# Performance work log

Hardware: AMD Instinct MI355X
Metric: run time of the kernel (lower is better)

The kernel has to match this reference:

```python
import jax, jax.numpy as jnp
import numpy as np

PARTS = (0.0, 0.25, 0.5, 0.75, 1.0)
N = 16777216


def setup_inputs() -> dict:
    key = jax.random.key(0)
    kx, ky, kd = jax.random.split(key, 3)
    x = jax.random.normal(kx, (N, 2), dtype=jnp.float32)
    y = jax.random.normal(ky, (N, 2), dtype=jnp.float32)
    dist = jax.random.uniform(kd, (N,), dtype=jnp.float32)
    return {"x": x, "y": y, "dist": dist}


def _complex_abs(v):
    # fastmri.complex_abs: sqrt(re^2 + im^2) over last dim of size 2
    return jnp.sqrt(jnp.sum(v * v, axis=-1))


def reference(x, y, dist):
    # Per-element squared errors computed once, then masked-reduced per radial bin.
    diff2_sum = jnp.sum((x - y) ** 2, axis=-1)        # [N] sum over the 2 components
    abs_diff2 = (_complex_abs(x) - _complex_abs(y)) ** 2  # [N]

    loss = jnp.float32(0.0)
    for i in range(len(PARTS) - 1):
        r0, r1 = PARTS[i], PARTS[i + 1]
        mask = (dist >= r0) & (dist <= r1)            # inclusive both ends, as in torch code
        cnt = jnp.sum(mask)                           # number of selected points
        # mse over x[ind] of shape [cnt, 2] -> divide by 2*cnt elements
        mse = jnp.sum(jnp.where(mask, diff2_sum, 0.0)) / jnp.maximum(2 * cnt, 1)
        mse_abs = jnp.sum(jnp.where(mask, abs_diff2, 0.0)) / jnp.maximum(cnt, 1)
        loss = loss + jnp.where(cnt > 0, mse + 0.1 * mse_abs, 0.0)
    return loss
```

## Files before the change

kernel.cpp:

```cpp
#include <hip/hip_runtime.h>

#define NBINS 4
#define BLOCK 256
#define WAVES_PER_BLOCK (BLOCK / 64)
#define NBLOCKS 2048

struct WS {
    float sum_v[NBINS];
    float cnt[NBINS];
};

__device__ __forceinline__ void accum_point(float x0, float x1, float y0, float y1,
                                            float d,
                                            float (&acc)[NBINS], float (&cnt)[NBINS]) {
    float sx = fmaf(x1, x1, x0 * x0);
    float sy = fmaf(y1, y1, y0 * y0);
    float dx0 = x0 - y0, dx1 = x1 - y1;
    float d2 = fmaf(dx1, dx1, dx0 * dx0);
    float t = __builtin_amdgcn_sqrtf(sx * sy);
    float ad2 = sx + sy - 2.0f * t;
    float v = fmaf(0.1f, ad2, 0.5f * d2);
    bool c1 = d < 0.25f;
    bool c2 = d < 0.5f;
    bool c3 = d < 0.75f;
    float m0 = c1 ? 1.0f : 0.0f;
    float m1 = (c2 && !c1) ? 1.0f : 0.0f;
    float m2 = (c3 && !c2) ? 1.0f : 0.0f;
    float m3 = c3 ? 0.0f : 1.0f;
    acc[0] = fmaf(v, m0, acc[0]);
    acc[1] = fmaf(v, m1, acc[1]);
    acc[2] = fmaf(v, m2, acc[2]);
    acc[3] = fmaf(v, m3, acc[3]);
    cnt[0] += m0;
    cnt[1] += m1;
    cnt[2] += m2;
    cnt[3] += m3;
}

__device__ __forceinline__ void accum2(const float4& xv, const float4& yv,
                                       const float2& dv,
                                       float (&acc)[NBINS], float (&cnt)[NBINS]) {
    accum_point(xv.x, xv.y, yv.x, yv.y, dv.x, acc, cnt);
    accum_point(xv.z, xv.w, yv.z, yv.w, dv.y, acc, cnt);
}

__global__ __launch_bounds__(BLOCK, 4) void radial_loss_main(
    const float* __restrict__ x, const float* __restrict__ y,
    const float* __restrict__ dist, WS* __restrict__ ws, int n) {
    float acc[NBINS] = {0.f, 0.f, 0.f, 0.f};
    float cnt[NBINS] = {0.f, 0.f, 0.f, 0.f};

    const int n2 = n >> 1;
    const float4* __restrict__ x4 = (const float4*)x;
    const float4* __restrict__ y4 = (const float4*)y;
    const float2* __restrict__ dd = (const float2*)dist;

    const int stride = NBLOCKS * BLOCK;
    const int nfull = n2 / stride;
    int i = blockIdx.x * BLOCK + threadIdx.x;

    float4 xa, ya, xb, yb;
    float2 da, db;
    if (nfull >= 1) { xa = x4[i]; ya = y4[i]; da = dd[i]; }
    if (nfull >= 2) { xb = x4[i + stride]; yb = y4[i + stride]; db = dd[i + stride]; }
#pragma unroll 2
    for (int k = 0; k + 2 < nfull; ++k) {
        float4 xc = x4[i + 2 * stride];
        float4 yc = y4[i + 2 * stride];
        float2 dc = dd[i + 2 * stride];
        accum2(xa, ya, da, acc, cnt);
        xa = xb; ya = yb; da = db;
        xb = xc; yb = yc; db = dc;
        i += stride;
    }
    if (nfull >= 2) {
        accum2(xa, ya, da, acc, cnt);
        xa = xb; ya = yb; da = db;
        i += stride;
    }
    if (nfull >= 1) {
        accum2(xa, ya, da, acc, cnt);
        i += stride;
    }
    if (i < n2) {
        accum2(x4[i], y4[i], dd[i], acc, cnt);
    }
    if (blockIdx.x == 0) {
        for (int p = (n2 << 1) + threadIdx.x; p < n; p += BLOCK) {
            accum_point(x[2 * p], x[2 * p + 1], y[2 * p], y[2 * p + 1], dist[p],
                        acc, cnt);
        }
    }

#pragma unroll
    for (int off = 32; off > 0; off >>= 1) {
#pragma unroll
        for (int b = 0; b < NBINS; ++b) {
            acc[b] += __shfl_down(acc[b], off);
            cnt[b] += __shfl_down(cnt[b], off);
        }
    }

    __shared__ float sm_v[WAVES_PER_BLOCK][NBINS];
    __shared__ float sm_c[WAVES_PER_BLOCK][NBINS];
    const int wave = threadIdx.x >> 6;
    const int lane = threadIdx.x & 63;
    if (lane == 0) {
#pragma unroll
        for (int b = 0; b < NBINS; ++b) {
            sm_v[wave][b] = acc[b];
            sm_c[wave][b] = cnt[b];
        }
    }
    __syncthreads();
    if (threadIdx.x < NBINS) {
        const int b = threadIdx.x;
        float tv = 0.f, tc = 0.f;
#pragma unroll
        for (int w = 0; w < WAVES_PER_BLOCK; ++w) {
            tv += sm_v[w][b];
            tc += sm_c[w][b];
        }
        atomicAdd(&ws->sum_v[b], tv);
        atomicAdd(&ws->cnt[b], tc);
    }
}

__global__ void radial_loss_final(const WS* __restrict__ ws, float* __restrict__ out) {
    if (threadIdx.x == 0 && blockIdx.x == 0) {
        float loss = 0.f;
#pragma unroll
        for (int b = 0; b < NBINS; ++b) {
            float c = ws->cnt[b];
            if (c > 0.f) loss += ws->sum_v[b] / c;
        }
        out[0] = loss;
    }
}

extern "C" void kernel_launch(void* const* d_in, const int* in_sizes, int n_in,
                              void* d_out, int out_size, void* d_ws, size_t ws_size,
                              hipStream_t stream) {
    const float* x = (const float*)d_in[0];
    const float* y = (const float*)d_in[1];
    const float* dist = (const float*)d_in[2];
    float* out = (float*)d_out;
    WS* ws = (WS*)d_ws;
    const int n = in_sizes[2];

    hipMemsetAsync(ws, 0, sizeof(WS), stream);
    radial_loss_main<<<NBLOCKS, BLOCK, 0, stream>>>(x, y, dist, ws, n);
    radial_loss_final<<<1, 64, 0, stream>>>(ws, out);
}
```

Before: 326.2 us.

## Deepen load pipeline with inline-asm global loads and explicit vmcnt waits

Replaces the compiler-scheduled two-deep prefetch with a four-stage software pipeline. The loads are written in inline assembly and followed by explicit s_waitcnt vmcnt counters and scheduling barriers, so more memory requests stay in flight per thread in this bandwidth-bound reduction. The fast path only runs when the per-thread iteration count is at least 8 and divisible by 4, which holds here (n2=8M, stride=512K, nfull=16). It adds register pressure and relies on hand-counted vmcnt values, which would be unsafe if the compiler emitted other memory ops inside the loop.

```diff
diff --git a/kernel.cpp b/kernel.cpp
--- a/kernel.cpp
+++ b/kernel.cpp
@@ -4,6 +4,9 @@
 #define BLOCK 256
 #define WAVES_PER_BLOCK (BLOCK / 64)
 #define NBLOCKS 2048
+
+typedef float f32x4 __attribute__((ext_vector_type(4)));
+typedef float f32x2 __attribute__((ext_vector_type(2)));
 
 struct WS {
     float sum_v[NBINS];
@@ -37,6 +40,13 @@
     cnt[3] += m3;
 }
 
+__device__ __forceinline__ void accum2v(const f32x4 xv, const f32x4 yv,
+                                        const f32x2 dv,
+                                        float (&acc)[NBINS], float (&cnt)[NBINS]) {
+    accum_point(xv.x, xv.y, yv.x, yv.y, dv.x, acc, cnt);
+    accum_point(xv.z, xv.w, yv.z, yv.w, dv.y, acc, cnt);
+}
+
 __device__ __forceinline__ void accum2(const float4& xv, const float4& yv,
                                        const float2& dv,
                                        float (&acc)[NBINS], float (&cnt)[NBINS]) {
@@ -44,6 +54,16 @@
     accum_point(xv.z, xv.w, yv.z, yv.w, dv.y, acc, cnt);
 }
 
+#define GLOAD4(dst, base, off) \
+    asm volatile("global_load_dwordx4 %0, %1, %2" : "=v"(dst) : "v"(off), "s"(base))
+#define GLOAD2(dst, base, off) \
+    asm volatile("global_load_dwordx2 %0, %1, %2" : "=v"(dst) : "v"(off), "s"(base))
+#define VWAIT(n)                                             \
+    do {                                                     \
+        asm volatile("s_waitcnt vmcnt(" #n ")" ::: "memory"); \
+        __builtin_amdgcn_sched_barrier(0);                   \
+    } while (0)
+
 __global__ __launch_bounds__(BLOCK, 4) void radial_loss_main(
     const float* __restrict__ x, const float* __restrict__ y,
     const float* __restrict__ dist, WS* __restrict__ ws, int n) {
@@ -51,38 +71,71 @@
     float cnt[NBINS] = {0.f, 0.f, 0.f, 0.f};
 
     const int n2 = n >> 1;
-    const float4* __restrict__ x4 = (const float4*)x;
-    const float4* __restrict__ y4 = (const float4*)y;
-    const float2* __restrict__ dd = (const float2*)dist;
-
     const int stride = NBLOCKS * BLOCK;
     const int nfull = n2 / stride;
     int i = blockIdx.x * BLOCK + threadIdx.x;
 
-    float4 xa, ya, xb, yb;
-    float2 da, db;
-    if (nfull >= 1) { xa = x4[i]; ya = y4[i]; da = dd[i]; }
-    if (nfull >= 2) { xb = x4[i + stride]; yb = y4[i + stride]; db = dd[i + stride]; }
-#pragma unroll 2
-    for (int k = 0; k + 2 < nfull; ++k) {
-        float4 xc = x4[i + 2 * stride];
-        float4 yc = y4[i + 2 * stride];
-        float2 dc = dd[i + 2 * stride];
-        accum2(xa, ya, da, acc, cnt);
-        xa = xb; ya = yb; da = db;
-        xb = xc; yb = yc; db = dc;
-        i += stride;
-    }
-    if (nfull >= 2) {
-        accum2(xa, ya, da, acc, cnt);
-        xa = xb; ya = yb; da = db;
-        i += stride;
-    }
-    if (nfull >= 1) {
-        accum2(xa, ya, da, acc, cnt);
-        i += stride;
-    }
+    if (nfull >= 8 && (nfull & 3) == 0) {
+        f32x4 x0, y0, x1, y1, x2, y2, x3, y3;
+        f32x2 d0, d1, d2, d3;
+#define ISSUE(j, idx)                                       \
+    do {                                                    \
+        unsigned o16 = (unsigned)(idx) * 16u;               \
+        unsigned o8 = (unsigned)(idx) * 8u;                 \
+        GLOAD4(x##j, x, o16);                               \
+        GLOAD4(y##j, y, o16);                               \
+        GLOAD2(d##j, dist, o8);                             \
+    } while (0)
+        ISSUE(0, i);
+        ISSUE(1, i + stride);
+        ISSUE(2, i + 2 * stride);
+        ISSUE(3, i + 3 * stride);
+        int k = 0;
+        for (; k + 8 <= nfull; k += 4) {
+            VWAIT(9); accum2v(x0, y0, d0, acc, cnt); ISSUE(0, i + 4 * stride);
+            VWAIT(9); accum2v(x1, y1, d1, acc, cnt); ISSUE(1, i + 5 * stride);
+            VWAIT(9); accum2v(x2, y2, d2, acc, cnt); ISSUE(2, i + 6 * stride);
+            VWAIT(9); accum2v(x3, y3, d3, acc, cnt); ISSUE(3, i + 7 * stride);
+            i += 4 * stride;
+        }
+        VWAIT(9); accum2v(x0, y0, d0, acc, cnt);
+        VWAIT(6); accum2v(x1, y1, d1, acc, cnt);
+        VWAIT(3); accum2v(x2, y2, d2, acc, cnt);
+        VWAIT(0); accum2v(x3, y3, d3, acc, cnt);
+        i += 4 * stride;
+#undef ISSUE
+    } else {
+        const float4* __restrict__ x4 = (const float4*)x;
+        const float4* __restrict__ y4 = (const float4*)y;
+        const float2* __restrict__ dd = (const float2*)dist;
+        float4 xa, ya, xb, yb;
+        float2 da, db;
+        if (nfull >= 1) { xa = x4[i]; ya = y4[i]; da = dd[i]; }
+        if (nfull >= 2) { xb = x4[i + stride]; yb = y4[i + stride]; db = dd[i + stride]; }
+        for (int k = 0; k + 2 < nfull; ++k) {
+            float4 xc = x4[i + 2 * stride];
+            float4 yc = y4[i + 2 * stride];
+            float2 dc = dd[i + 2 * stride];
+            accum2(xa, ya, da, acc, cnt);
+            xa = xb; ya = yb; da = db;
+            xb = xc; yb = yc; db = dc;
+            i += stride;
+        }
+        if (nfull >= 2) {
+            accum2(xa, ya, da, acc, cnt);
+            xa = xb; ya = yb; da = db;
+            i += stride;
+        }
+        if (nfull >= 1) {
+            accum2(xa, ya, da, acc, cnt);
+            i += stride;
+        }
+    }
+
     if (i < n2) {
+        const float4* __restrict__ x4 = (const float4*)x;
+        const float4* __restrict__ y4 = (const float4*)y;
+        const float2* __restrict__ dd = (const float2*)dist;
         accum2(x4[i], y4[i], dd[i], acc, cnt);
     }
     if (blockIdx.x == 0) {
```

After: 320.3 us. Within noise of the previous version (-1.8%).

## Stream inputs through LDS with async global_load_lds double buffering

Applied to the files above, without the earlier changes.

The main loop now stages x, y and dist through per-wave LDS slices using global_load_lds direct-to-LDS loads, double-buffered with explicit vmcnt waits, in place of register-prefetched float4 loads. Each wave step handles 4 points per lane, and the tail is processed with a strided scalar loop. The aim is to keep more bytes in flight and reduce VGPR pressure in this bandwidth-bound reduction. In exchange it adds LDS traffic, a 40KB shared allocation that may limit occupancy, and fragile hand-set waitcnt ordering.

```diff
diff --git a/kernel.cpp b/kernel.cpp
--- a/kernel.cpp
+++ b/kernel.cpp
@@ -4,6 +4,11 @@
 #define BLOCK 256
 #define WAVES_PER_BLOCK (BLOCK / 64)
 #define NBLOCKS 2048
+#define SLICE_BYTES 5120
+#define BUF_BYTES (WAVES_PER_BLOCK * SLICE_BYTES)
+#define PTS_PER_STEP (NBLOCKS * BLOCK * 4)
+
+typedef float f32x4 __attribute__((ext_vector_type(4)));
 
 struct WS {
     float sum_v[NBINS];
@@ -37,59 +42,70 @@
     cnt[3] += m3;
 }
 
-__device__ __forceinline__ void accum2(const float4& xv, const float4& yv,
-                                       const float2& dv,
-                                       float (&acc)[NBINS], float (&cnt)[NBINS]) {
-    accum_point(xv.x, xv.y, yv.x, yv.y, dv.x, acc, cnt);
-    accum_point(xv.z, xv.w, yv.z, yv.w, dv.y, acc, cnt);
-}
+#define GLDS(gaddr, laddr)                                                        \
+    __builtin_amdgcn_global_load_lds(                                             \
+        (const __attribute__((address_space(1))) void*)(gaddr),                   \
+        (__attribute__((address_space(3))) void*)(laddr), 16, 0, 0)
 
 __global__ __launch_bounds__(BLOCK, 4) void radial_loss_main(
     const float* __restrict__ x, const float* __restrict__ y,
     const float* __restrict__ dist, WS* __restrict__ ws, int n) {
+    __shared__ __align__(16) char smem[2 * BUF_BYTES];
+
     float acc[NBINS] = {0.f, 0.f, 0.f, 0.f};
     float cnt[NBINS] = {0.f, 0.f, 0.f, 0.f};
 
-    const int n2 = n >> 1;
-    const float4* __restrict__ x4 = (const float4*)x;
-    const float4* __restrict__ y4 = (const float4*)y;
-    const float2* __restrict__ dd = (const float2*)dist;
+    const int w = threadIdx.x >> 6;
+    const int l = threadIdx.x & 63;
+    const int nsteps = n / PTS_PER_STEP;
 
-    const int stride = NBLOCKS * BLOCK;
-    const int nfull = n2 / stride;
-    int i = blockIdx.x * BLOCK + threadIdx.x;
+    char* slice0 = smem + w * SLICE_BYTES;
+    char* slice1 = smem + BUF_BYTES + w * SLICE_BYTES;
 
-    float4 xa, ya, xb, yb;
-    float2 da, db;
-    if (nfull >= 1) { xa = x4[i]; ya = y4[i]; da = dd[i]; }
-    if (nfull >= 2) { xb = x4[i + stride]; yb = y4[i + stride]; db = dd[i + stride]; }
-#pragma unroll 2
-    for (int k = 0; k + 2 < nfull; ++k) {
-        float4 xc = x4[i + 2 * stride];
-        float4 yc = y4[i + 2 * stride];
-        float2 dc = dd[i + 2 * stride];
-        accum2(xa, ya, da, acc, cnt);
-        xa = xb; ya = yb; da = db;
-        xb = xc; yb = yc; db = dc;
-        i += stride;
+    auto issue = [&](int t, char* slice) {
+        const int ptb = (t * NBLOCKS + blockIdx.x) * (BLOCK * 4) + w * 256;
+        const char* xs = (const char*)x + (size_t)ptb * 8;
+        const char* ys = (const char*)y + (size_t)ptb * 8;
+        const char* ds = (const char*)dist + (size_t)ptb * 4;
+        GLDS(xs + l * 16, slice);
+        GLDS(xs + 1024 + l * 16, slice + 1024);
+        GLDS(ys + l * 16, slice + 2048);
+        GLDS(ys + 1024 + l * 16, slice + 3072);
+        GLDS(ds + l * 16, slice + 4096);
+    };
+
+    auto consume = [&](const char* slice) {
+        f32x4 xv0 = *(const f32x4*)(slice + 32 * l);
+        f32x4 xv1 = *(const f32x4*)(slice + 32 * l + 16);
+        f32x4 yv0 = *(const f32x4*)(slice + 2048 + 32 * l);
+        f32x4 yv1 = *(const f32x4*)(slice + 2048 + 32 * l + 16);
+        f32x4 dv = *(const f32x4*)(slice + 4096 + 16 * l);
+        accum_point(xv0.x, xv0.y, yv0.x, yv0.y, dv.x, acc, cnt);
+        accum_point(xv0.z, xv0.w, yv0.z, yv0.w, dv.y, acc, cnt);
+        accum_point(xv1.x, xv1.y, yv1.x, yv1.y, dv.z, acc, cnt);
+        accum_point(xv1.z, xv1.w, yv1.z, yv1.w, dv.w, acc, cnt);
+    };
+
+    if (nsteps >= 1) {
+        issue(0, slice0);
+        char* cur = slice0;
+        char* nxt = slice1;
+        for (int t = 0; t + 1 < nsteps; ++t) {
+            issue(t + 1, nxt);
+            asm volatile("s_waitcnt vmcnt(5)" ::: "memory");
+            __builtin_amdgcn_sched_barrier(0);
+            consume(cur);
+            char* tmp = cur; cur = nxt; nxt = tmp;
+        }
+        asm volatile("s_waitcnt vmcnt(0)" ::: "memory");
+        __builtin_amdgcn_sched_barrier(0);
+        consume(cur);
     }
-    if (nfull >= 2) {
-        accum2(xa, ya, da, acc, cnt);
-        xa = xb; ya = yb; da = db;
-        i += stride;
-    }
-    if (nfull >= 1) {
-        accum2(xa, ya, da, acc, cnt);
-        i += stride;
-    }
-    if (i < n2) {
-        accum2(x4[i], y4[i], dd[i], acc, cnt);
-    }
-    if (blockIdx.x == 0) {
-        for (int p = (n2 << 1) + threadIdx.x; p < n; p += BLOCK) {
-            accum_point(x[2 * p], x[2 * p + 1], y[2 * p], y[2 * p + 1], dist[p],
-                        acc, cnt);
-        }
+
+    for (int p = nsteps * PTS_PER_STEP + blockIdx.x * BLOCK + threadIdx.x; p < n;
+         p += NBLOCKS * BLOCK) {
+        accum_point(x[2 * p], x[2 * p + 1], y[2 * p], y[2 * p + 1], dist[p], acc,
+                    cnt);
     }
 
 #pragma unroll
@@ -101,15 +117,14 @@
         }
     }
 
-    __shared__ float sm_v[WAVES_PER_BLOCK][NBINS];
-    __shared__ float sm_c[WAVES_PER_BLOCK][NBINS];
-    const int wave = threadIdx.x >> 6;
-    const int lane = threadIdx.x & 63;
-    if (lane == 0) {
+    __syncthreads();
+    float* sm_v = (float*)smem;
+    float* sm_c = sm_v + WAVES_PER_BLOCK * NBINS;
+    if (l == 0) {
 #pragma unroll
         for (int b = 0; b < NBINS; ++b) {
-            sm_v[wave][b] = acc[b];
-            sm_c[wave][b] = cnt[b];
+            sm_v[w * NBINS + b] = acc[b];
+            sm_c[w * NBINS + b] = cnt[b];
         }
     }
     __syncthreads();
@@ -117,9 +132,9 @@
         const int b = threadIdx.x;
         float tv = 0.f, tc = 0.f;
 #pragma unroll
-        for (int w = 0; w < WAVES_PER_BLOCK; ++w) {
-            tv += sm_v[w][b];
-            tc += sm_c[w][b];
+        for (int wv = 0; wv < WAVES_PER_BLOCK; ++wv) {
+            tv += sm_v[wv * NBINS + b];
+            tc += sm_c[wv * NBINS + b];
         }
         atomicAdd(&ws->sum_v[b], tv);
         atomicAdd(&ws->cnt[b], tc);
```

New measurement: 321.4 us. Within noise of the previous version (-1.5%).
